# Kernel optimization log

Hardware: AMD Instinct MI355X
Metric: run time of the kernel (lower is better)

Reference implementation:

```python
import jax, jax.numpy as jnp
import numpy as np

H = 1024          # frame height (template.shape[0])
W = 1024          # frame width  (template.shape[1])
CD = 900          # center_dims
MS = 10           # ms_h = ms_w
EPS = 1e-8
CS = (H - CD) // 2        # c_shp_x = c_shp_y = 62
OFF = MS + CS             # template crop offset = 72
TW = H - 2 * OFF          # cropped template side = 880
S = 2 * MS + 1            # NCC map side = 21


def setup_inputs() -> dict:
    key = jax.random.key(0)
    k1, k2 = jax.random.split(key)
    # spatially-correlated synthetic frame so the NCC peak is real (log-peak interpolation valid)
    noise = jax.random.normal(k1, (1, H, W, 1), jnp.float32)
    smooth = jax.lax.reduce_window(noise, 0.0, jax.lax.add, (1, 15, 15, 1), (1, 1, 1, 1), 'SAME') / 225.0
    template = smooth[0, :, :, 0]
    X = jnp.roll(template, (3, -2), axis=(0, 1))[None, :, :, None] \
        + 0.05 * jax.random.normal(k2, (1, H, W, 1), jnp.float32)
    return {"X": X, "template": template}


def _forward(X, template):
    # --- template normalization (zero-mean, variance) ---
    tmpl = template[OFF:H - OFF, OFF:W - OFF]                  # (TW, TW)
    t_zm = tmpl - jnp.mean(tmpl)
    t_var = jnp.sum(t_zm * t_zm) + EPS                         # scalar

    # --- image local normalization over the template window ---
    Xc = X[:, CS:H - CS, CS:W - CS, :]                         # (1, CD, CD, 1)
    imgs_zm = Xc - jnp.mean(Xc, axis=(1, 2), keepdims=True)
    win = (1, TW, TW, 1)
    ls = jax.lax.reduce_window(Xc, 0.0, jax.lax.add, win, (1, 1, 1, 1), 'VALID')        # local sum  (1,S,S,1)
    lsq = jax.lax.reduce_window(Xc * Xc, 0.0, jax.lax.add, win, (1, 1, 1, 1), 'VALID')  # local sumsq
    var = lsq - ls * ls / (TW * TW) + EPS
    var = jnp.maximum(var, 0.0)

    # --- NCC numerator: correlate zero-mean image with zero-mean template ---
    num = jax.lax.conv_general_dilated(
        imgs_zm, t_zm[:, :, None, None], (1, 1), 'VALID',
        dimension_numbers=('NHWC', 'HWIO', 'NHWC'))           # (1, S, S, 1)
    ncc = num / jnp.sqrt(t_var * var)
    ncc = jnp.where(jnp.isnan(ncc), 0.0, ncc)

    # --- subpixel peak via log-Gaussian interpolation ---
    ncc2 = ncc[0, :, :, 0]                                     # (S, S)
    idx = jnp.argmax(ncc2.reshape(-1))
    sx = (idx // S).astype(jnp.int32)
    sy = (idx % S).astype(jnp.int32)
    lg = jnp.log(ncc2)

    def at(r, c):
        return lg[jnp.clip(r, 0, S - 1), jnp.clip(c, 0, S - 1)]

    l_xm1, l_xp1 = at(sx - 1, sy), at(sx + 1, sy)
    l_ym1, l_yp1 = at(sx, sy - 1), at(sx, sy + 1)
    l4 = 4.0 * at(sx, sy)
    xs = -(sx.astype(jnp.float32) - MS) - (l_xm1 - l_xp1) / (2 * l_xm1 - l4 + 2 * l_xp1)
    ys = -(sy.astype(jnp.float32) - MS) - (l_ym1 - l_yp1) / (2 * l_ym1 - l4 + 2 * l_yp1)

    # --- bilinear translate (tfa.image.translate semantics: out[r,c] = in[r-xs, c-ys], fill 0) ---
    img = X[0, :, :, 0]
    rr = jnp.arange(H, dtype=jnp.float32) - xs
    cc = jnp.arange(W, dtype=jnp.float32) - ys
    r0 = jnp.floor(rr)
    c0 = jnp.floor(cc)
    wr = (rr - r0)[:, None]
    wc = (cc - c0)[None, :]
    r0i = r0.astype(jnp.int32)
    c0i = c0.astype(jnp.int32)

    def samp(ri, ci):
        vr = ((ri >= 0) & (ri < H))[:, None]
        vc = ((ci >= 0) & (ci < W))[None, :]
        v = img[jnp.clip(ri, 0, H - 1)[:, None], jnp.clip(ci, 0, W - 1)[None, :]]
        return jnp.where(vr & vc, v, 0.0)

    out = ((1 - wr) * (1 - wc) * samp(r0i, c0i)
           + (1 - wr) * wc * samp(r0i, c0i + 1)
           + wr * (1 - wc) * samp(r0i + 1, c0i)
           + wr * wc * samp(r0i + 1, c0i + 1))                 # (H, W)

    flat = out.T.reshape(-1)[None, :]                          # matches reshape(transpose(squeeze(.)), [-1])[None,:]
    return flat, xs, ys


def reference(X, template):
    flat, xs, ys = _forward(X, template)
    return (flat, xs, ys)
```

## Files before the change

### kernel.cpp

```cpp
#include <hip/hip_runtime.h>
#include <math.h>

#define HH 1024
#define WW 1024
#define CD 900
#define MS 10
#define CS 62
#define OFFT 72
#define TW 880
#define SS 21
#define EPSV 1e-8
#define NBAND 55
#define RPB 16
#define NCH 55
#define NPAIR 441
#define NIG 7
#define IPG 3
#define AROWS 18
#define NCORR (NBAND * NIG)


__global__ __launch_bounds__(256) void fused_corr_stats(const float* __restrict__ X,
                                                        const float* __restrict__ T,
                                                        float* __restrict__ RS1T,
                                                        float* __restrict__ RS2T,
                                                        float* __restrict__ Trow1,
                                                        float* __restrict__ Trow2,
                                                        float* __restrict__ Sfull,
                                                        float* __restrict__ part) {
    const int bx = blockIdx.x;
    const int tid = threadIdx.x;
    const int lane = tid & 63, wid = tid >> 6;
    __shared__ float red[4][IPG * SS];

    if (bx < NCORR) {
        const int g = bx / NBAND;
        const int band = bx - g * NBAND;
        const int i0 = g * IPG;
        const int u0 = band * RPB;

        float acc[IPG][SS];
#pragma unroll
        for (int d = 0; d < IPG; ++d)
#pragma unroll
            for (int j = 0; j < SS; ++j) acc[d][j] = 0.f;

#pragma unroll 1
        for (int item = tid; item < AROWS * NCH; item += 256) {
            const int a = item / NCH;
            const int c = item - a * NCH;
            const float4* xp = (const float4*)(X + (size_t)(CS + i0 + u0 + a) * WW + 60 + c * 16);
            float xr[40];
#pragma unroll
            for (int k = 0; k < 10; ++k) {
                float4 q = xp[k];
                xr[4 * k] = q.x; xr[4 * k + 1] = q.y; xr[4 * k + 2] = q.z; xr[4 * k + 3] = q.w;
            }
#pragma unroll
            for (int d = 0; d < IPG; ++d) {
                const int u = a - d;
                if (u >= 0 && u < RPB) {
                    const float4* tp = (const float4*)(T + (size_t)(OFFT + u0 + u) * WW + OFFT + c * 16);
                    float t[16];
#pragma unroll
                    for (int k = 0; k < 4; ++k) {
                        float4 q = tp[k];
                        t[4 * k] = q.x; t[4 * k + 1] = q.y; t[4 * k + 2] = q.z; t[4 * k + 3] = q.w;
                    }
#pragma unroll
                    for (int j = 0; j < SS; ++j) {
                        float s = acc[d][j];
#pragma unroll
                        for (int k = 0; k < 16; ++k) s = fmaf(xr[2 + j + k], t[k], s);
                        acc[d][j] = s;
                    }
                }
            }
        }

#pragma unroll
        for (int d = 0; d < IPG; ++d)
#pragma unroll
            for (int j = 0; j < SS; ++j)
#pragma unroll
                for (int m = 1; m < 64; m <<= 1) acc[d][j] += __shfl_xor(acc[d][j], m);

        if (lane == 0) {
#pragma unroll
            for (int d = 0; d < IPG; ++d)
#pragma unroll
                for (int j = 0; j < SS; ++j) red[wid][d * SS + j] = acc[d][j];
        }
        __syncthreads();
        if (tid < IPG * SS) {
            const int d = tid / SS, j = tid - d * SS;
            float s = red[0][tid] + red[1][tid] + red[2][tid] + red[3][tid];
            part[((i0 + d) * NBAND + band) * SS + j] = s;
        }
    } else {
        const int b = bx - NCORR;
        if (b < CD) {
            const float* row = X + (size_t)(CS + b) * WW + CS;
            float sf = 0.f, sw = 0.f, qw = 0.f;
            for (int v = tid; v < CD; v += 256) {
                float x = row[v];
                sf += x;
                if (v < TW) { sw += x; qw += x * x; }
            }
            for (int m = 1; m < 64; m <<= 1) {
                sf += __shfl_xor(sf, m); sw += __shfl_xor(sw, m); qw += __shfl_xor(qw, m);
            }
            if (lane == 0) { red[wid][0] = sf; red[wid][1] = sw; red[wid][2] = qw; }
            __syncthreads();
            if (tid < 32) {
                const float swb = red[0][1] + red[1][1] + red[2][1] + red[3][1];
                const float qwb = red[0][2] + red[1][2] + red[2][2] + red[3][2];
                float d1 = 0.f, d2 = 0.f;
                if (tid >= 1 && tid < SS) {
                    float a = row[tid - 1], c2 = row[TW + tid - 1];
                    d1 = c2 - a;
                    d2 = c2 * c2 - a * a;
                }
                for (int off = 1; off < 32; off <<= 1) {
                    float u1 = __shfl_up(d1, off), u2 = __shfl_up(d2, off);
                    if (tid >= off) { d1 += u1; d2 += u2; }
                }
                if (tid < SS) {
                    RS1T[tid * CD + b] = swb + d1;
                    RS2T[tid * CD + b] = qwb + d2;
                }
                if (tid == 0) Sfull[b] = red[0][0] + red[1][0] + red[2][0] + red[3][0];
            }
        } else {
            const int u = b - CD;
            const float* row = T + (size_t)(OFFT + u) * WW + OFFT;
            float s = 0.f, q = 0.f;
            for (int v = tid; v < TW; v += 256) { float t = row[v]; s += t; q += t * t; }
            for (int m = 1; m < 64; m <<= 1) { s += __shfl_xor(s, m); q += __shfl_xor(q, m); }
            if (lane == 0) { red[wid][0] = s; red[wid][1] = q; }
            __syncthreads();
            if (tid == 0) {
                Trow1[u] = red[0][0] + red[1][0] + red[2][0] + red[3][0];
                Trow2[u] = red[0][1] + red[1][1] + red[2][1] + red[3][1];
            }
        }
    }
}

__global__ __launch_bounds__(256) void ncc_final_kernel(const float* __restrict__ part,
                                                        const float* __restrict__ RS1T,
                                                        const float* __restrict__ RS2T,
                                                        const float* __restrict__ Trow1,
                                                        const float* __restrict__ Trow2,
                                                        const float* __restrict__ Sfull,
                                                        float* __restrict__ ncc) {
    const int bid = blockIdx.x;
    const int i = bid / SS, j = bid - i * SS;
    const int tid = threadIdx.x;
    double dd = 0, d1 = 0, d2 = 0, ta = 0, tb = 0, xs = 0;
    for (int b = tid; b < NBAND; b += 256) dd += (double)part[(i * NBAND + b) * SS + j];
    const float* r1 = RS1T + j * CD + i;
    const float* r2 = RS2T + j * CD + i;
    for (int u = tid; u < TW; u += 256) {
        d1 += (double)r1[u]; d2 += (double)r2[u];
        ta += (double)Trow1[u]; tb += (double)Trow2[u];
    }
    for (int k = tid; k < CD; k += 256) xs += (double)Sfull[k];
    for (int m = 1; m < 64; m <<= 1) {
        dd += __shfl_xor(dd, m); d1 += __shfl_xor(d1, m); d2 += __shfl_xor(d2, m);
        ta += __shfl_xor(ta, m); tb += __shfl_xor(tb, m); xs += __shfl_xor(xs, m);
    }
    __shared__ double red[4][6];
    const int lane = tid & 63, wid = tid >> 6;
    if (lane == 0) {
        red[wid][0] = dd; red[wid][1] = d1; red[wid][2] = d2;
        red[wid][3] = ta; red[wid][4] = tb; red[wid][5] = xs;
    }
    __syncthreads();
    if (tid == 0) {
        double dot = red[0][0] + red[1][0] + red[2][0] + red[3][0];
        double S1  = red[0][1] + red[1][1] + red[2][1] + red[3][1];
        double S2  = red[0][2] + red[1][2] + red[2][2] + red[3][2];
        double sum_t  = red[0][3] + red[1][3] + red[2][3] + red[3][3];
        double sum_t2 = red[0][4] + red[1][4] + red[2][4] + red[3][4];
        double sumX   = red[0][5] + red[1][5] + red[2][5] + red[3][5];
        const double NT = 774400.0;
        double mt = sum_t / NT, mx = sumX / 810000.0;
        double tvar = sum_t2 - sum_t * sum_t / NT + EPSV;
        double var = S2 - S1 * S1 / NT + EPSV;
        if (var < 0.0) var = 0.0;
        double cross = dot - mt * S1 - mx * sum_t + NT * mx * mt;
        float val = (float)(cross / sqrt(tvar * var));
        if (isnan(val)) val = 0.f;
        ncc[i * SS + j] = val;
    }
}

__global__ __launch_bounds__(256) void shift_kernel(const float* __restrict__ img,
                                                    const float* __restrict__ ncc,
                                                    float* __restrict__ out) {
    __shared__ float sv[256];
    __shared__ int si[256];
    __shared__ float sxy[2];
    __shared__ float tile[64][65];
    const int tid = threadIdx.x;

    {
        float v = -1e30f; int vi = 0;
        for (int k = tid; k < SS * SS; k += 256) {
            float q = ncc[k];
            if (q > v) { v = q; vi = k; }
        }
        sv[tid] = v; si[tid] = vi;
        __syncthreads();
        for (int off = 128; off > 0; off >>= 1) {
            if (tid < off) {
                float v2 = sv[tid + off]; int i2 = si[tid + off];
                if (v2 > sv[tid] || (v2 == sv[tid] && i2 < si[tid])) { sv[tid] = v2; si[tid] = i2; }
            }
            __syncthreads();
        }
        if (tid == 0) {
            int idx = si[0];
            int sx = idx / SS;
            int sy = idx - sx * SS;
            auto at = [&](int r, int c) -> float {
                r = r < 0 ? 0 : (r > SS - 1 ? SS - 1 : r);
                c = c < 0 ? 0 : (c > SS - 1 ? SS - 1 : c);
                return logf(ncc[r * SS + c]);
            };
            float l4 = 4.0f * at(sx, sy);
            float lxm = at(sx - 1, sy), lxp = at(sx + 1, sy);
            float lym = at(sx, sy - 1), lyp = at(sx, sy + 1);
            float xsv = -((float)sx - (float)MS) - (lxm - lxp) / (2.0f * lxm - l4 + 2.0f * lxp);
            float ysv = -((float)sy - (float)MS) - (lym - lyp) / (2.0f * lym - l4 + 2.0f * lyp);
            sxy[0] = xsv; sxy[1] = ysv;
            if (blockIdx.x == 0 && blockIdx.y == 0) {
                out[(size_t)HH * WW] = xsv;
                out[(size_t)HH * WW + 1] = ysv;
            }
        }
        __syncthreads();
    }

    const float xs = sxy[0], ys = sxy[1];
    const int R0 = blockIdx.y * 64, C0 = blockIdx.x * 64;
    {
        const int cl = tid & 63, rg = tid >> 6;
        const int c = C0 + cl;
        const float cc = (float)c - ys;
        const float c0f = floorf(cc);
        const float wc = cc - c0f;
        const int c0 = (int)c0f;
        const bool vc0 = (c0 >= 0) & (c0 < WW);
        const bool vc1 = (c0 + 1 >= 0) & (c0 + 1 < WW);
        const int c0c = c0 < 0 ? 0 : (c0 > WW - 1 ? WW - 1 : c0);
        const int c1c = (c0 + 1) < 0 ? 0 : ((c0 + 1) > WW - 1 ? WW - 1 : c0 + 1);
        for (int k = 0; k < 16; ++k) {
            const int rl = rg * 16 + k;
            const int r = R0 + rl;
            const float rr = (float)r - xs;
            const float r0f = floorf(rr);
            const float wr = rr - r0f;
            const int r0 = (int)r0f;
            const bool vr0 = (r0 >= 0) & (r0 < HH);
            const bool vr1 = (r0 + 1 >= 0) & (r0 + 1 < HH);
            const int r0c = r0 < 0 ? 0 : (r0 > HH - 1 ? HH - 1 : r0);
            const int r1c = (r0 + 1) < 0 ? 0 : ((r0 + 1) > HH - 1 ? HH - 1 : r0 + 1);
            float s00 = img[(size_t)r0c * WW + c0c]; if (!(vr0 & vc0)) s00 = 0.f;
            float s01 = img[(size_t)r0c * WW + c1c]; if (!(vr0 & vc1)) s01 = 0.f;
            float s10 = img[(size_t)r1c * WW + c0c]; if (!(vr1 & vc0)) s10 = 0.f;
            float s11 = img[(size_t)r1c * WW + c1c]; if (!(vr1 & vc1)) s11 = 0.f;
            tile[rl][cl] = (1.f - wr) * (1.f - wc) * s00 + (1.f - wr) * wc * s01 +
                           wr * (1.f - wc) * s10 + wr * wc * s11;
        }
    }
    __syncthreads();
    {
        const int rl = tid & 63, cg = tid >> 6;
        for (int k = 0; k < 16; ++k) {
            const int cl = cg * 16 + k;
            out[(size_t)(C0 + cl) * HH + R0 + rl] = tile[rl][cl];
        }
    }
}

extern "C" void kernel_launch(void* const* d_in, const int* in_sizes, int n_in,
                              void* d_out, int out_size, void* d_ws, size_t ws_size,
                              hipStream_t stream) {
    const float* X = (const float*)d_in[0];
    const float* T = (const float*)d_in[1];
    float* out = (float*)d_out;

    char* w = (char*)d_ws;
    float* RS1T  = (float*)(w + 0);
    float* RS2T  = (float*)(w + 75600);
    float* Trow1 = (float*)(w + 151200);
    float* Trow2 = (float*)(w + 154720);
    float* Sfull = (float*)(w + 158240);
    float* part  = (float*)(w + 161840);
    float* ncc   = (float*)(w + 258880);

    fused_corr_stats<<<NCORR + CD + TW, 256, 0, stream>>>(X, T, RS1T, RS2T, Trow1, Trow2, Sfull, part);
    ncc_final_kernel<<<SS * SS, 256, 0, stream>>>(part, RS1T, RS2T, Trow1, Trow2, Sfull, ncc);
    shift_kernel<<<dim3(16, 16), 256, 0, stream>>>(X, ncc, out);
}
```

Baseline: 93.93 us.

## Fuse NCC finalization into shift kernel with sliding-window row sums

Drops the separate NCC-final kernel launch. Every shift block now recomputes the 21x21 NCC map itself in shared memory. The per-column local sums come from an initial full row-sum per column followed by a sliding-window update (add the entering value, subtract the leaving one), rather than 880-element reductions for every pair. This saves one launch and the global round-trip of the ncc map, but repeats the small NCC computation in all 256 blocks and serializes the prefix update over 21 threads.

```diff
diff --git a/kernel.cpp b/kernel.cpp
--- a/kernel.cpp
+++ b/kernel.cpp
@@ -147,101 +147,121 @@
     }
 }
 
-__global__ __launch_bounds__(256) void ncc_final_kernel(const float* __restrict__ part,
+__global__ __launch_bounds__(256) void ncc_shift_kernel(const float* __restrict__ img,
+                                                        const float* __restrict__ part,
                                                         const float* __restrict__ RS1T,
                                                         const float* __restrict__ RS2T,
                                                         const float* __restrict__ Trow1,
                                                         const float* __restrict__ Trow2,
                                                         const float* __restrict__ Sfull,
-                                                        float* __restrict__ ncc) {
-    const int bid = blockIdx.x;
-    const int i = bid / SS, j = bid - i * SS;
-    const int tid = threadIdx.x;
-    double dd = 0, d1 = 0, d2 = 0, ta = 0, tb = 0, xs = 0;
-    for (int b = tid; b < NBAND; b += 256) dd += (double)part[(i * NBAND + b) * SS + j];
-    const float* r1 = RS1T + j * CD + i;
-    const float* r2 = RS2T + j * CD + i;
-    for (int u = tid; u < TW; u += 256) {
-        d1 += (double)r1[u]; d2 += (double)r2[u];
-        ta += (double)Trow1[u]; tb += (double)Trow2[u];
-    }
-    for (int k = tid; k < CD; k += 256) xs += (double)Sfull[k];
-    for (int m = 1; m < 64; m <<= 1) {
-        dd += __shfl_xor(dd, m); d1 += __shfl_xor(d1, m); d2 += __shfl_xor(d2, m);
-        ta += __shfl_xor(ta, m); tb += __shfl_xor(tb, m); xs += __shfl_xor(xs, m);
-    }
-    __shared__ double red[4][6];
-    const int lane = tid & 63, wid = tid >> 6;
-    if (lane == 0) {
-        red[wid][0] = dd; red[wid][1] = d1; red[wid][2] = d2;
-        red[wid][3] = ta; red[wid][4] = tb; red[wid][5] = xs;
-    }
-    __syncthreads();
-    if (tid == 0) {
-        double dot = red[0][0] + red[1][0] + red[2][0] + red[3][0];
-        double S1  = red[0][1] + red[1][1] + red[2][1] + red[3][1];
-        double S2  = red[0][2] + red[1][2] + red[2][2] + red[3][2];
-        double sum_t  = red[0][3] + red[1][3] + red[2][3] + red[3][3];
-        double sum_t2 = red[0][4] + red[1][4] + red[2][4] + red[3][4];
-        double sumX   = red[0][5] + red[1][5] + red[2][5] + red[3][5];
-        const double NT = 774400.0;
-        double mt = sum_t / NT, mx = sumX / 810000.0;
-        double tvar = sum_t2 - sum_t * sum_t / NT + EPSV;
-        double var = S2 - S1 * S1 / NT + EPSV;
-        if (var < 0.0) var = 0.0;
-        double cross = dot - mt * S1 - mx * sum_t + NT * mx * mt;
-        float val = (float)(cross / sqrt(tvar * var));
-        if (isnan(val)) val = 0.f;
-        ncc[i * SS + j] = val;
-    }
-}
-
-__global__ __launch_bounds__(256) void shift_kernel(const float* __restrict__ img,
-                                                    const float* __restrict__ ncc,
-                                                    float* __restrict__ out) {
+                                                        float* __restrict__ out) {
+    const int tid = threadIdx.x, lane = tid & 63, wid = tid >> 6;
+    __shared__ double sh_b1[SS], sh_b2[SS];
+    __shared__ double sh_dot[NPAIR];
+    __shared__ double sh_d1[420], sh_d2[420];
+    __shared__ double sh_S1[NPAIR], sh_S2[NPAIR];
+    __shared__ double redsc[4][3];
+    __shared__ double sh_scal[3];
+    __shared__ float nccs[NPAIR];
     __shared__ float sv[256];
     __shared__ int si[256];
     __shared__ float sxy[2];
     __shared__ float tile[64][65];
-    const int tid = threadIdx.x;
-
+
+    for (int j = wid; j < SS; j += 4) {
+        const float* r1 = RS1T + j * CD;
+        const float* r2 = RS2T + j * CD;
+        double s1 = 0, s2 = 0;
+        for (int u = lane; u < TW; u += 64) { s1 += (double)r1[u]; s2 += (double)r2[u]; }
+        for (int m = 1; m < 64; m <<= 1) { s1 += __shfl_xor(s1, m); s2 += __shfl_xor(s2, m); }
+        if (lane == 0) { sh_b1[j] = s1; sh_b2[j] = s2; }
+    }
     {
-        float v = -1e30f; int vi = 0;
-        for (int k = tid; k < SS * SS; k += 256) {
-            float q = ncc[k];
-            if (q > v) { v = q; vi = k; }
-        }
-        sv[tid] = v; si[tid] = vi;
+        double ta = 0, tb = 0, xsum = 0;
+        for (int u = tid; u < TW; u += 256) { ta += (double)Trow1[u]; tb += (double)Trow2[u]; }
+        for (int k = tid; k < CD; k += 256) xsum += (double)Sfull[k];
+        for (int m = 1; m < 64; m <<= 1) {
+            ta += __shfl_xor(ta, m); tb += __shfl_xor(tb, m); xsum += __shfl_xor(xsum, m);
+        }
+        if (lane == 0) { redsc[wid][0] = ta; redsc[wid][1] = tb; redsc[wid][2] = xsum; }
+    }
+    for (int p = tid; p < NPAIR; p += 256) {
+        const int i = p / SS, j = p - i * SS;
+        double dv = 0;
+        for (int b = 0; b < NBAND; ++b) dv += (double)part[(i * NBAND + b) * SS + j];
+        sh_dot[p] = dv;
+    }
+    for (int q = tid; q < 420; q += 256) {
+        const int ii = q / SS + 1;
+        const int j = q - (ii - 1) * SS;
+        sh_d1[q] = (double)RS1T[j * CD + ii + 879] - (double)RS1T[j * CD + ii - 1];
+        sh_d2[q] = (double)RS2T[j * CD + ii + 879] - (double)RS2T[j * CD + ii - 1];
+    }
+    __syncthreads();
+
+    if (tid < SS) {
+        const int j = tid;
+        double w1 = sh_b1[j], w2 = sh_b2[j];
+        sh_S1[j] = w1; sh_S2[j] = w2;
+        for (int i2 = 1; i2 < SS; ++i2) {
+            w1 += sh_d1[(i2 - 1) * SS + j];
+            w2 += sh_d2[(i2 - 1) * SS + j];
+            sh_S1[i2 * SS + j] = w1;
+            sh_S2[i2 * SS + j] = w2;
+        }
+    } else if (tid >= 32 && tid < 35) {
+        const int s = tid - 32;
+        sh_scal[s] = redsc[0][s] + redsc[1][s] + redsc[2][s] + redsc[3][s];
+    }
+    __syncthreads();
+
+    {
+        float best = -1e30f; int bi = 0;
+        const double NT = 774400.0;
+        const double sum_t = sh_scal[0], sum_t2 = sh_scal[1], sumX = sh_scal[2];
+        const double mt = sum_t / NT, mx = sumX / 810000.0;
+        const double tvar = sum_t2 - sum_t * sum_t / NT + EPSV;
+        for (int p = tid; p < NPAIR; p += 256) {
+            const double dot = sh_dot[p], S1 = sh_S1[p], S2 = sh_S2[p];
+            double var = S2 - S1 * S1 / NT + EPSV;
+            if (var < 0.0) var = 0.0;
+            const double cross = dot - mt * S1 - mx * sum_t + NT * mx * mt;
+            float v = (float)(cross / sqrt(tvar * var));
+            if (isnan(v)) v = 0.f;
+            nccs[p] = v;
+            if (v > best) { best = v; bi = p; }
+        }
+        sv[tid] = best; si[tid] = bi;
+    }
+    __syncthreads();
+    for (int off = 128; off > 0; off >>= 1) {
+        if (tid < off) {
+            float v2 = sv[tid + off]; int i2 = si[tid + off];
+            if (v2 > sv[tid] || (v2 == sv[tid] && i2 < si[tid])) { sv[tid] = v2; si[tid] = i2; }
+        }
         __syncthreads();
-        for (int off = 128; off > 0; off >>= 1) {
-            if (tid < off) {
-                float v2 = sv[tid + off]; int i2 = si[tid + off];
-                if (v2 > sv[tid] || (v2 == sv[tid] && i2 < si[tid])) { sv[tid] = v2; si[tid] = i2; }
-            }
-            __syncthreads();
-        }
-        if (tid == 0) {
-            int idx = si[0];
-            int sx = idx / SS;
-            int sy = idx - sx * SS;
-            auto at = [&](int r, int c) -> float {
-                r = r < 0 ? 0 : (r > SS - 1 ? SS - 1 : r);
-                c = c < 0 ? 0 : (c > SS - 1 ? SS - 1 : c);
-                return logf(ncc[r * SS + c]);
-            };
-            float l4 = 4.0f * at(sx, sy);
-            float lxm = at(sx - 1, sy), lxp = at(sx + 1, sy);
-            float lym = at(sx, sy - 1), lyp = at(sx, sy + 1);
-            float xsv = -((float)sx - (float)MS) - (lxm - lxp) / (2.0f * lxm - l4 + 2.0f * lxp);
-            float ysv = -((float)sy - (float)MS) - (lym - lyp) / (2.0f * lym - l4 + 2.0f * lyp);
-            sxy[0] = xsv; sxy[1] = ysv;
-            if (blockIdx.x == 0 && blockIdx.y == 0) {
-                out[(size_t)HH * WW] = xsv;
-                out[(size_t)HH * WW + 1] = ysv;
-            }
-        }
-        __syncthreads();
-    }
+    }
+    if (tid == 0) {
+        const int idx = si[0];
+        const int sx = idx / SS;
+        const int sy = idx - sx * SS;
+        auto at = [&](int r, int c) -> float {
+            r = r < 0 ? 0 : (r > SS - 1 ? SS - 1 : r);
+            c = c < 0 ? 0 : (c > SS - 1 ? SS - 1 : c);
+            return logf(nccs[r * SS + c]);
+        };
+        const float l4 = 4.0f * at(sx, sy);
+        const float lxm = at(sx - 1, sy), lxp = at(sx + 1, sy);
+        const float lym = at(sx, sy - 1), lyp = at(sx, sy + 1);
+        const float xsv = -((float)sx - (float)MS) - (lxm - lxp) / (2.0f * lxm - l4 + 2.0f * lxp);
+        const float ysv = -((float)sy - (float)MS) - (lym - lyp) / (2.0f * lym - l4 + 2.0f * lyp);
+        sxy[0] = xsv; sxy[1] = ysv;
+        if (blockIdx.x == 0 && blockIdx.y == 0) {
+            out[(size_t)HH * WW] = xsv;
+            out[(size_t)HH * WW + 1] = ysv;
+        }
+    }
+    __syncthreads();
 
     const float xs = sxy[0], ys = sxy[1];
     const int R0 = blockIdx.y * 64, C0 = blockIdx.x * 64;
@@ -299,9 +319,7 @@
     float* Trow2 = (float*)(w + 154720);
     float* Sfull = (float*)(w + 158240);
     float* part  = (float*)(w + 161840);
-    float* ncc   = (float*)(w + 258880);
 
     fused_corr_stats<<<NCORR + CD + TW, 256, 0, stream>>>(X, T, RS1T, RS2T, Trow1, Trow2, Sfull, part);
-    ncc_final_kernel<<<SS * SS, 256, 0, stream>>>(part, RS1T, RS2T, Trow1, Trow2, Sfull, ncc);
-    shift_kernel<<<dim3(16, 16), 256, 0, stream>>>(X, ncc, out);
+    ncc_shift_kernel<<<dim3(16, 16), 256, 0, stream>>>(X, part, RS1T, RS2T, Trow1, Trow2, Sfull, out);
 }
```

New measurement: 121.8 us. 1.3x slower.
